# Kernel tuning notes

Measured on AMD Instinct MI355X. Metric: run time of the kernel, lower is better.

Reference implementation:

```python
import jax, jax.numpy as jnp
import numpy as np

N_NODES = 100000
N_EDGES = 1000000
N_PAIRS = 2000000
IN_CH = 64
OUT_CH = 64
NODE_DIM = 37
STATE_DIM = 5


def setup_inputs() -> dict:
    key = jax.random.key(0)
    ks = jax.random.split(key, 8)
    fan_edge = NODE_DIM + IN_CH + STATE_DIM  # 106, glorot scale
    s_edge = (6.0 / (fan_edge + OUT_CH)) ** 0.5
    s_e = (6.0 / (IN_CH + OUT_CH)) ** 0.5
    return {
        "x": jax.random.normal(ks[0], (N_NODES, NODE_DIM), jnp.float32),
        "global_state": jax.random.normal(ks[1], (N_NODES, STATE_DIM), jnp.float32),
        "edge_attr": jax.random.normal(ks[2], (N_EDGES, IN_CH), jnp.float32),
        "W_edge": jax.random.uniform(ks[3], (OUT_CH, fan_edge), jnp.float32, -s_edge, s_edge),
        "b_edge": jnp.zeros((OUT_CH,), jnp.float32),
        "W_e": jax.random.uniform(ks[4], (OUT_CH, IN_CH), jnp.float32, -s_e, s_e),
        "b_e": jnp.zeros((OUT_CH,), jnp.float32),
        "atom_index": jax.random.randint(ks[5], (2, N_PAIRS), 0, N_NODES, jnp.int64 if jax.config.read('jax_enable_x64') else jnp.int32),
        "e_idx": jax.random.randint(ks[6], (2, N_PAIRS), 0, N_EDGES, jnp.int64 if jax.config.read('jax_enable_x64') else jnp.int32),
    }


def reference(x, global_state, edge_attr, W_edge, b_edge, W_e, b_e, atom_index, e_idx):
    # x: [N, node_dim] -> concat global state: [N, node_dim+state_dim]
    xg = jnp.concatenate([x, global_state], axis=1)
    # gather edge and node features along the edge-adjacency (line graph) pairs
    feat = jnp.concatenate([edge_attr[e_idx[1]], xg[atom_index[0]]], axis=-1)  # [K, 106]
    h = jax.nn.elu(feat @ W_edge.T + b_edge)  # [K, out]
    # scatter-add into per-edge accumulator of E rows
    edge_out = jax.ops.segment_sum(h, e_idx[0], num_segments=edge_attr.shape[0])
    return jax.nn.elu(edge_attr @ W_e.T + b_e) + edge_out
```

## Files before the change

kernel.cpp:

```cpp
#include <hip/hip_runtime.h>

#define N_NODES   100000
#define N_EDGES   1000000
#define N_PAIRS   2000000
#define IN_CH     64
#define OUT_CH    64
#define NODE_DIM  37
#define STATE_DIM 5
#define FEAT_DIM  106

__device__ __forceinline__ float elu_f(float s) {
    return s > 0.f ? s : expm1f(s);
}

__global__ __launch_bounds__(256, 4) void base_kernel(
    const float* __restrict__ ea,
    const float* __restrict__ We,
    const float* __restrict__ be,
    float* __restrict__ out)
{
    const int t    = threadIdx.x;
    const int wave = __builtin_amdgcn_readfirstlane(t >> 6);
    const int lane = t & 63;

    float wrow[IN_CH];
    #pragma unroll
    for (int j = 0; j < IN_CH; ++j)
        wrow[j] = We[lane * IN_CH + j];
    const float bias = be[lane];

    const int gw  = blockIdx.x * 4 + wave;
    const int gws = gridDim.x * 4;
    for (int e = gw * 2; e < N_EDGES; e += gws * 2) {
        const float4* r0 = (const float4*)(ea + (size_t)e * IN_CH);
        const float4* r1 = (const float4*)(ea + (size_t)(e + 1) * IN_CH);
        float a0 = bias, a1 = 0.f, a2 = 0.f, a3 = 0.f;
        float b0 = bias, b1 = 0.f, b2 = 0.f, b3 = 0.f;
        #pragma unroll
        for (int q = 0; q < IN_CH / 4; ++q) {
            const float4 f = r0[q];
            const float4 g = r1[q];
            a0 = fmaf(wrow[4 * q + 0], f.x, a0);
            a1 = fmaf(wrow[4 * q + 1], f.y, a1);
            a2 = fmaf(wrow[4 * q + 2], f.z, a2);
            a3 = fmaf(wrow[4 * q + 3], f.w, a3);
            b0 = fmaf(wrow[4 * q + 0], g.x, b0);
            b1 = fmaf(wrow[4 * q + 1], g.y, b1);
            b2 = fmaf(wrow[4 * q + 2], g.z, b2);
            b3 = fmaf(wrow[4 * q + 3], g.w, b3);
        }
        out[(size_t)e * OUT_CH + lane]       = elu_f((a0 + a1) + (a2 + a3));
        out[(size_t)(e + 1) * OUT_CH + lane] = elu_f((b0 + b1) + (b2 + b3));
    }
}

__global__ __launch_bounds__(256, 2) void pair_kernel(
    const float* __restrict__ x,
    const float* __restrict__ gs,
    const float* __restrict__ ea,
    const float* __restrict__ W,
    const float* __restrict__ b,
    const int* __restrict__ aidx,
    const int* __restrict__ eidx,
    float* __restrict__ out)
{
    const int t    = threadIdx.x;
    const int wave = __builtin_amdgcn_readfirstlane(t >> 6);
    const int lane = t & 63;

    float wrow[FEAT_DIM];
    #pragma unroll
    for (int j = 0; j < FEAT_DIM; ++j)
        wrow[j] = W[lane * FEAT_DIM + j];
    const float bias = b[lane];

    const int gw  = blockIdx.x * 4 + wave;
    const int gws = gridDim.x * 4;
    for (int k = gw * 2; k < N_PAIRS; k += gws * 2) {
        const int segA = eidx[k];
        const int segB = eidx[k + 1];
        const int e2A  = eidx[N_PAIRS + k];
        const int e2B  = eidx[N_PAIRS + k + 1];
        const int a0A  = aidx[k];
        const int a0B  = aidx[k + 1];

        const float4* rA = (const float4*)(ea + (size_t)e2A * IN_CH);
        const float4* rB = (const float4*)(ea + (size_t)e2B * IN_CH);
        const float*  xA = x  + (size_t)a0A * NODE_DIM;
        const float*  xB = x  + (size_t)a0B * NODE_DIM;
        const float*  gA = gs + (size_t)a0A * STATE_DIM;
        const float*  gB = gs + (size_t)a0B * STATE_DIM;

        float sA0 = bias, sA1 = 0.f, sA2 = 0.f, sA3 = 0.f;
        float sB0 = bias, sB1 = 0.f, sB2 = 0.f, sB3 = 0.f;

        #pragma unroll
        for (int q = 0; q < IN_CH / 4; ++q) {
            const float4 f = rA[q];
            const float4 g = rB[q];
            sA0 = fmaf(wrow[4 * q + 0], f.x, sA0);
            sA1 = fmaf(wrow[4 * q + 1], f.y, sA1);
            sA2 = fmaf(wrow[4 * q + 2], f.z, sA2);
            sA3 = fmaf(wrow[4 * q + 3], f.w, sA3);
            sB0 = fmaf(wrow[4 * q + 0], g.x, sB0);
            sB1 = fmaf(wrow[4 * q + 1], g.y, sB1);
            sB2 = fmaf(wrow[4 * q + 2], g.z, sB2);
            sB3 = fmaf(wrow[4 * q + 3], g.w, sB3);
        }
        #pragma unroll
        for (int j = 0; j < 36; j += 4) {
            sA0 = fmaf(wrow[IN_CH + j + 0], xA[j + 0], sA0);
            sA1 = fmaf(wrow[IN_CH + j + 1], xA[j + 1], sA1);
            sA2 = fmaf(wrow[IN_CH + j + 2], xA[j + 2], sA2);
            sA3 = fmaf(wrow[IN_CH + j + 3], xA[j + 3], sA3);
            sB0 = fmaf(wrow[IN_CH + j + 0], xB[j + 0], sB0);
            sB1 = fmaf(wrow[IN_CH + j + 1], xB[j + 1], sB1);
            sB2 = fmaf(wrow[IN_CH + j + 2], xB[j + 2], sB2);
            sB3 = fmaf(wrow[IN_CH + j + 3], xB[j + 3], sB3);
        }
        sA0 = fmaf(wrow[IN_CH + 36], xA[36], sA0);
        sB0 = fmaf(wrow[IN_CH + 36], xB[36], sB0);
        #pragma unroll
        for (int j = 0; j < STATE_DIM; ++j) {
            sA1 = fmaf(wrow[IN_CH + NODE_DIM + j], gA[j], sA1);
            sB1 = fmaf(wrow[IN_CH + NODE_DIM + j], gB[j], sB1);
        }

        const float hA = elu_f((sA0 + sA1) + (sA2 + sA3));
        const float hB = elu_f((sB0 + sB1) + (sB2 + sB3));
        atomicAdd(&out[(size_t)segA * OUT_CH + lane], hA);
        atomicAdd(&out[(size_t)segB * OUT_CH + lane], hB);
    }
}

extern "C" void kernel_launch(void* const* d_in, const int* in_sizes, int n_in,
                              void* d_out, int out_size, void* d_ws, size_t ws_size,
                              hipStream_t stream) {
    const float* x    = (const float*)d_in[0];
    const float* gs   = (const float*)d_in[1];
    const float* ea   = (const float*)d_in[2];
    const float* W    = (const float*)d_in[3];
    const float* b    = (const float*)d_in[4];
    const float* We   = (const float*)d_in[5];
    const float* be   = (const float*)d_in[6];
    const int*   aidx = (const int*)d_in[7];
    const int*   eidx = (const int*)d_in[8];
    float* out = (float*)d_out;

    base_kernel<<<2048, 256, 0, stream>>>(ea, We, be, out);
    pair_kernel<<<2048, 256, 0, stream>>>(x, gs, ea, W, b, aidx, eidx, out);
}
```

Before: 2.142 ms.

## Map lanes to pairs and edges with scalar-loaded weights, chunked channels

Both kernels are restructured so that each lane processes one pair (or one edge) instead of one output channel. Output channels are walked in chunks of 16 accumulators, with weight reads made wave-uniform so they can come through scalar loads. This is meant to cut per-lane weight register pressure and raise occupancy. The cost is that each lane now gathers its own feature row, re-reading it once per chunk, and issues atomics and stores to scattered rows instead of one contiguous 256-byte row per wave, which risks heavily uncoalesced memory traffic.

```diff
diff --git a/kernel.cpp b/kernel.cpp
--- a/kernel.cpp
+++ b/kernel.cpp
@@ -13,48 +13,7 @@
     return s > 0.f ? s : expm1f(s);
 }
 
-__global__ __launch_bounds__(256, 4) void base_kernel(
-    const float* __restrict__ ea,
-    const float* __restrict__ We,
-    const float* __restrict__ be,
-    float* __restrict__ out)
-{
-    const int t    = threadIdx.x;
-    const int wave = __builtin_amdgcn_readfirstlane(t >> 6);
-    const int lane = t & 63;
-
-    float wrow[IN_CH];
-    #pragma unroll
-    for (int j = 0; j < IN_CH; ++j)
-        wrow[j] = We[lane * IN_CH + j];
-    const float bias = be[lane];
-
-    const int gw  = blockIdx.x * 4 + wave;
-    const int gws = gridDim.x * 4;
-    for (int e = gw * 2; e < N_EDGES; e += gws * 2) {
-        const float4* r0 = (const float4*)(ea + (size_t)e * IN_CH);
-        const float4* r1 = (const float4*)(ea + (size_t)(e + 1) * IN_CH);
-        float a0 = bias, a1 = 0.f, a2 = 0.f, a3 = 0.f;
-        float b0 = bias, b1 = 0.f, b2 = 0.f, b3 = 0.f;
-        #pragma unroll
-        for (int q = 0; q < IN_CH / 4; ++q) {
-            const float4 f = r0[q];
-            const float4 g = r1[q];
-            a0 = fmaf(wrow[4 * q + 0], f.x, a0);
-            a1 = fmaf(wrow[4 * q + 1], f.y, a1);
-            a2 = fmaf(wrow[4 * q + 2], f.z, a2);
-            a3 = fmaf(wrow[4 * q + 3], f.w, a3);
-            b0 = fmaf(wrow[4 * q + 0], g.x, b0);
-            b1 = fmaf(wrow[4 * q + 1], g.y, b1);
-            b2 = fmaf(wrow[4 * q + 2], g.z, b2);
-            b3 = fmaf(wrow[4 * q + 3], g.w, b3);
-        }
-        out[(size_t)e * OUT_CH + lane]       = elu_f((a0 + a1) + (a2 + a3));
-        out[(size_t)(e + 1) * OUT_CH + lane] = elu_f((b0 + b1) + (b2 + b3));
-    }
-}
-
-__global__ __launch_bounds__(256, 2) void pair_kernel(
+__global__ __launch_bounds__(256, 4) void pair_kernel(
     const float* __restrict__ x,
     const float* __restrict__ gs,
     const float* __restrict__ ea,
@@ -65,71 +24,125 @@
     float* __restrict__ out)
 {
     const int t    = threadIdx.x;
-    const int wave = __builtin_amdgcn_readfirstlane(t >> 6);
     const int lane = t & 63;
+    const int wid  = blockIdx.x * 4 + (t >> 6);
+    const int nw   = gridDim.x * 4;
 
-    float wrow[FEAT_DIM];
-    #pragma unroll
-    for (int j = 0; j < FEAT_DIM; ++j)
-        wrow[j] = W[lane * FEAT_DIM + j];
-    const float bias = b[lane];
+    for (int base = wid * 64; base < N_PAIRS; base += nw * 64) {
+        const int  k     = base + lane;
+        const bool valid = k < N_PAIRS;
+        const int  kc    = valid ? k : N_PAIRS - 1;
 
-    const int gw  = blockIdx.x * 4 + wave;
-    const int gws = gridDim.x * 4;
-    for (int k = gw * 2; k < N_PAIRS; k += gws * 2) {
-        const int segA = eidx[k];
-        const int segB = eidx[k + 1];
-        const int e2A  = eidx[N_PAIRS + k];
-        const int e2B  = eidx[N_PAIRS + k + 1];
-        const int a0A  = aidx[k];
-        const int a0B  = aidx[k + 1];
+        const int seg = eidx[kc];
+        const int e2  = eidx[N_PAIRS + kc];
+        const int a0  = aidx[kc];
 
-        const float4* rA = (const float4*)(ea + (size_t)e2A * IN_CH);
-        const float4* rB = (const float4*)(ea + (size_t)e2B * IN_CH);
-        const float*  xA = x  + (size_t)a0A * NODE_DIM;
-        const float*  xB = x  + (size_t)a0B * NODE_DIM;
-        const float*  gA = gs + (size_t)a0A * STATE_DIM;
-        const float*  gB = gs + (size_t)a0B * STATE_DIM;
+        const float* er = ea + (size_t)e2 * IN_CH;
+        const float* xr = x  + (size_t)a0 * NODE_DIM;
+        const float* gr = gs + (size_t)a0 * STATE_DIM;
 
-        float sA0 = bias, sA1 = 0.f, sA2 = 0.f, sA3 = 0.f;
-        float sB0 = bias, sB1 = 0.f, sB2 = 0.f, sB3 = 0.f;
+        #pragma unroll 1
+        for (int c0 = 0; c0 < OUT_CH; c0 += 16) {
+            float acc[16];
+            #pragma unroll
+            for (int cc = 0; cc < 16; ++cc)
+                acc[cc] = b[c0 + cc];
 
-        #pragma unroll
-        for (int q = 0; q < IN_CH / 4; ++q) {
-            const float4 f = rA[q];
-            const float4 g = rB[q];
-            sA0 = fmaf(wrow[4 * q + 0], f.x, sA0);
-            sA1 = fmaf(wrow[4 * q + 1], f.y, sA1);
-            sA2 = fmaf(wrow[4 * q + 2], f.z, sA2);
-            sA3 = fmaf(wrow[4 * q + 3], f.w, sA3);
-            sB0 = fmaf(wrow[4 * q + 0], g.x, sB0);
-            sB1 = fmaf(wrow[4 * q + 1], g.y, sB1);
-            sB2 = fmaf(wrow[4 * q + 2], g.z, sB2);
-            sB3 = fmaf(wrow[4 * q + 3], g.w, sB3);
+            #pragma unroll
+            for (int jw = 0; jw < IN_CH / 4; ++jw) {
+                const float4 f = *(const float4*)(er + jw * 4);
+                #pragma unroll
+                for (int cc = 0; cc < 16; ++cc) {
+                    const float* wr = W + (size_t)(c0 + cc) * FEAT_DIM + jw * 4;
+                    acc[cc] = fmaf(f.x, wr[0], acc[cc]);
+                    acc[cc] = fmaf(f.y, wr[1], acc[cc]);
+                    acc[cc] = fmaf(f.z, wr[2], acc[cc]);
+                    acc[cc] = fmaf(f.w, wr[3], acc[cc]);
+                }
+            }
+            #pragma unroll
+            for (int jw = 0; jw < 9; ++jw) {
+                const float f0 = xr[jw * 4 + 0];
+                const float f1 = xr[jw * 4 + 1];
+                const float f2 = xr[jw * 4 + 2];
+                const float f3 = xr[jw * 4 + 3];
+                #pragma unroll
+                for (int cc = 0; cc < 16; ++cc) {
+                    const float* wr = W + (size_t)(c0 + cc) * FEAT_DIM + IN_CH + jw * 4;
+                    acc[cc] = fmaf(f0, wr[0], acc[cc]);
+                    acc[cc] = fmaf(f1, wr[1], acc[cc]);
+                    acc[cc] = fmaf(f2, wr[2], acc[cc]);
+                    acc[cc] = fmaf(f3, wr[3], acc[cc]);
+                }
+            }
+            {
+                const float f0 = xr[36];
+                const float g0 = gr[0], g1 = gr[1], g2 = gr[2];
+                const float g3 = gr[3], g4 = gr[4];
+                #pragma unroll
+                for (int cc = 0; cc < 16; ++cc) {
+                    const float* wr = W + (size_t)(c0 + cc) * FEAT_DIM + 100;
+                    acc[cc] = fmaf(f0, wr[0], acc[cc]);
+                    acc[cc] = fmaf(g0, wr[1], acc[cc]);
+                    acc[cc] = fmaf(g1, wr[2], acc[cc]);
+                    acc[cc] = fmaf(g2, wr[3], acc[cc]);
+                    acc[cc] = fmaf(g3, wr[4], acc[cc]);
+                    acc[cc] = fmaf(g4, wr[5], acc[cc]);
+                }
+            }
+
+            if (valid) {
+                #pragma unroll
+                for (int cc = 0; cc < 16; ++cc)
+                    atomicAdd(&out[(size_t)seg * OUT_CH + c0 + cc],
+                              elu_f(acc[cc]));
+            }
         }
-        #pragma unroll
-        for (int j = 0; j < 36; j += 4) {
-            sA0 = fmaf(wrow[IN_CH + j + 0], xA[j + 0], sA0);
-            sA1 = fmaf(wrow[IN_CH + j + 1], xA[j + 1], sA1);
-            sA2 = fmaf(wrow[IN_CH + j + 2], xA[j + 2], sA2);
-            sA3 = fmaf(wrow[IN_CH + j + 3], xA[j + 3], sA3);
-            sB0 = fmaf(wrow[IN_CH + j + 0], xB[j + 0], sB0);
-            sB1 = fmaf(wrow[IN_CH + j + 1], xB[j + 1], sB1);
-            sB2 = fmaf(wrow[IN_CH + j + 2], xB[j + 2], sB2);
-            sB3 = fmaf(wrow[IN_CH + j + 3], xB[j + 3], sB3);
+    }
+}
+
+__global__ __launch_bounds__(256, 4) void base_kernel(
+    const float* __restrict__ ea,
+    const float* __restrict__ We,
+    const float* __restrict__ be,
+    float* __restrict__ out)
+{
+    const int t    = threadIdx.x;
+    const int lane = t & 63;
+    const int wid  = blockIdx.x * 4 + (t >> 6);
+    const int nw   = gridDim.x * 4;
+
+    for (int base = wid * 64; base < N_EDGES; base += nw * 64) {
+        const int  e     = base + lane;
+        const bool valid = e < N_EDGES;
+        const int  ec    = valid ? e : N_EDGES - 1;
+        const float* er  = ea + (size_t)ec * IN_CH;
+
+        #pragma unroll 1
+        for (int c0 = 0; c0 < OUT_CH; c0 += 16) {
+            float acc[16];
+            #pragma unroll
+            for (int cc = 0; cc < 16; ++cc)
+                acc[cc] = be[c0 + cc];
+
+            #pragma unroll
+            for (int jw = 0; jw < IN_CH / 4; ++jw) {
+                const float4 f = *(const float4*)(er + jw * 4);
+                #pragma unroll
+                for (int cc = 0; cc < 16; ++cc) {
+                    const float* wr = We + (size_t)(c0 + cc) * IN_CH + jw * 4;
+                    acc[cc] = fmaf(f.x, wr[0], acc[cc]);
+                    acc[cc] = fmaf(f.y, wr[1], acc[cc]);
+                    acc[cc] = fmaf(f.z, wr[2], acc[cc]);
+                    acc[cc] = fmaf(f.w, wr[3], acc[cc]);
+                }
+            }
+            if (valid) {
+                #pragma unroll
+                for (int cc = 0; cc < 16; ++cc)
+                    out[(size_t)e * OUT_CH + c0 + cc] = elu_f(acc[cc]);
+            }
         }
-        sA0 = fmaf(wrow[IN_CH + 36], xA[36], sA0);
-        sB0 = fmaf(wrow[IN_CH + 36], xB[36], sB0);
-        #pragma unroll
-        for (int j = 0; j < STATE_DIM; ++j) {
-            sA1 = fmaf(wrow[IN_CH + NODE_DIM + j], gA[j], sA1);
-            sB1 = fmaf(wrow[IN_CH + NODE_DIM + j], gB[j], sB1);
-        }
-
-        const float hA = elu_f((sA0 + sA1) + (sA2 + sA3));
-        const float hB = elu_f((sB0 + sB1) + (sB2 + sB3));
-        atomicAdd(&out[(size_t)segA * OUT_CH + lane], hA);
-        atomicAdd(&out[(size_t)segB * OUT_CH + lane], hB);
     }
 }
 
```

Measured after the change: 7.465 ms. +248.5%, slower.
